# Kernel tuning notes

Measured on AMD Instinct MI355X. Metric: run time of the kernel, lower is better.

The kernel has to match this reference:

```python
import jax, jax.numpy as jnp
import numpy as np

D = 1280      # embed_dim
H = 20        # num_heads
HD = D // H   # head_dim = 64
B = 4         # batch (number of requests)
ENC = 1500    # encoder length per request (Whisper 30s)
KV = B * ENC  # 6000 packed cross kv tokens
SEQ = [300, 500, 350, 450]  # ragged decoder lengths, sum = 1600
Q = sum(SEQ)


def setup_inputs() -> dict:
    key = jax.random.key(0)
    ks = jax.random.split(key, 8)
    s = 0.02
    return {
        "hidden_states": jax.random.normal(ks[0], (Q, D), jnp.float32),
        "cross_hidden_states": jax.random.normal(ks[1], (KV, D), jnp.float32),
        "seq_lens": jnp.array(SEQ, dtype=jnp.int32),
        "Wq": jax.random.normal(ks[2], (D, D), jnp.float32) * s,
        "bq": jax.random.normal(ks[3], (D,), jnp.float32) * s,
        "Wkv": jax.random.normal(ks[4], (D, 2 * D), jnp.float32) * s,
        "bkv": jax.random.normal(ks[5], (2 * D,), jnp.float32) * s,
        "Wo": jax.random.normal(ks[6], (D, D), jnp.float32) * s,
        "bo": jax.random.normal(ks[7], (D,), jnp.float32) * s,
    }


def reference(hidden_states, cross_hidden_states, seq_lens, Wq, bq, Wkv, bkv, Wo, bo):
    q_len, d = hidden_states.shape
    kv_len = cross_hidden_states.shape[0]
    bsz = seq_lens.shape[0]
    enc_len = kv_len // bsz
    scaling = jnp.float32(HD) ** -0.5

    # projections (packed tokens)
    q = (hidden_states @ Wq + bq) * scaling           # [Q, D]
    kv = cross_hidden_states @ Wkv + bkv              # [KV, 2D]
    k, v = kv[:, :d], kv[:, d:]

    # [H, L, HD]
    qh = q.reshape(q_len, H, HD).transpose(1, 0, 2)
    kh = k.reshape(kv_len, H, HD).transpose(1, 0, 2)
    vh = v.reshape(kv_len, H, HD).transpose(1, 0, 2)

    scores = jnp.einsum("hqd,hkd->hqk", qh, kh)       # [H, Q, KV]

    # ragged block-diagonal mask: query token i belongs to request
    # searchsorted(cumsum(seq_lens), i, 'right'); kv token j to j // enc_len
    cum = jnp.cumsum(seq_lens)
    q_req = jnp.searchsorted(cum, jnp.arange(q_len), side="right")
    kv_req = jnp.arange(kv_len) // enc_len
    mask = q_req[:, None] == kv_req[None, :]          # [Q, KV] bool

    scores = jnp.where(mask[None, :, :], scores, -jnp.inf)
    probs = jax.nn.softmax(scores, axis=-1)
    attn = jnp.einsum("hqk,hkd->hqd", probs, vh)      # [H, Q, HD]
    attn = attn.transpose(1, 0, 2).reshape(q_len, d)
    return attn @ Wo + bo
```

## Files before the change

### kernel.cpp

```cpp
#include <hip/hip_runtime.h>
#include <stdint.h>

#define AS1 __attribute__((address_space(1)))
#define AS3 __attribute__((address_space(3)))

typedef __bf16 bf16_t;
typedef bf16_t bf16x8 __attribute__((ext_vector_type(8)));
typedef float  f32x4  __attribute__((ext_vector_type(4)));
typedef float  f32x16 __attribute__((ext_vector_type(16)));
typedef unsigned short u16;

constexpr int D     = 1280;
constexpr int H     = 20;
constexpr int HD    = 64;
constexpr int NQ    = 1600;
constexpr int NKV   = 6000;
constexpr int ENC   = 1500;
constexpr int QPAD  = 1632;
constexpr int KVP   = 1504;
constexpr int KVTOT = 4 * KVP;
constexpr int KB_PER_REQ = KVP / 32;
constexpr int KB_TOT     = 4 * KB_PER_REQ;

__device__ __forceinline__ u16 f2bf(float f) {
  union { float f; uint32_t u; } x; x.f = f;
  uint32_t r = (x.u + 0x7fffu + ((x.u >> 16) & 1u)) >> 16;
  return (u16)r;
}

__device__ __forceinline__ void gload16(const void* g, void* l) {
  __builtin_amdgcn_global_load_lds((AS1 void*)g, (AS3 void*)l, 16, 0, 0);
}

__device__ __forceinline__ void cvt_body(const float* __restrict__ in, u16* __restrict__ out,
                                         int i, int n4) {
  if (i >= n4) return;
  float4 v = ((const float4*)in)[i];
  ushort4 o;
  o.x = f2bf(v.x); o.y = f2bf(v.y); o.z = f2bf(v.z); o.w = f2bf(v.w);
  ((ushort4*)out)[i] = o;
}

__device__ __forceinline__ void tpose_body(const float* __restrict__ in, u16* __restrict__ out,
                                           int R, int C, int bx, int by, u16 (*tile)[33]) {
  int bc = bx * 32, br = by * 32;
  int tx = threadIdx.x & 31, ty = threadIdx.x >> 5;
#pragma unroll
  for (int i = 0; i < 32; i += 8)
    tile[ty + i][tx] = f2bf(in[(size_t)(br + ty + i) * C + bc + tx]);
  __syncthreads();
#pragma unroll
  for (int i = 0; i < 32; i += 8)
    out[(size_t)(bc + ty + i) * R + br + tx] = tile[tx][ty + i];
}

__global__ __launch_bounds__(256)
void prep_kernel(const float* __restrict__ hs, const float* __restrict__ chs,
                 const float* __restrict__ Wq, const float* __restrict__ Wkv,
                 const float* __restrict__ Wo,
                 u16* __restrict__ hsb, u16* __restrict__ chsb,
                 u16* __restrict__ Wqt, u16* __restrict__ Wkvt, u16* __restrict__ Wot) {
  __shared__ u16 tile[32][33];
  int b = blockIdx.x;
  if (b < 2000) {
    cvt_body(hs, hsb, b * 256 + threadIdx.x, 512000);
  } else if (b < 9500) {
    cvt_body(chs, chsb, (b - 2000) * 256 + threadIdx.x, 1920000);
  } else if (b < 11100) {
    int t = b - 9500;  tpose_body(Wq,  Wqt,  1280, 1280, t % 40, t / 40, tile);
  } else if (b < 14300) {
    int t = b - 11100; tpose_body(Wkv, Wkvt, 1280, 2560, t % 80, t / 80, tile);
  } else {
    int t = b - 14300; tpose_body(Wo,  Wot,  1280, 1280, t % 40, t / 40, tile);
  }
}

template <int MODE>
__device__ __forceinline__ void gemm_tile(
    int m0, int n0, const u16* __restrict__ A, const u16* __restrict__ Bt,
    const float* __restrict__ bias, int M,
    u16* __restrict__ outA, u16* __restrict__ outB, float* __restrict__ outF,
    u16* lds) {
  const int tid = threadIdx.x;
  const int lane = tid & 63, l15 = lane & 15, lg = lane >> 4;
  const int w = tid >> 6, wr = w >> 1, wc = w & 1;
  const bool vside = (MODE == 1) && (n0 >= D);
  constexpr int NT = D / 64;

  auto stage = [&](int tj, int c) {
    int buf = (tj & 1) * 32768;
    if (c < 4) {
      int off = c * 4096 + tid * 16;
      int loff = off ^ (((off >> 7) & 7) << 4);
      int row = loff >> 7, colb = loff & 127;
      int gr = m0 + row; gr = gr < M ? gr : M - 1;
      gload16((const char*)A + ((size_t)gr * D + tj * 64) * 2 + colb,
              (char*)lds + buf + off);
    } else {
      int off = (c - 4) * 4096 + tid * 16;
      int loff = off ^ (((off >> 7) & 7) << 4);
      int row = loff >> 7, colb = loff & 127;
      int gr = n0 + row;
      gload16((const char*)Bt + ((size_t)gr * D + tj * 64) * 2 + colb,
              (char*)lds + buf + 16384 + off);
    }
  };

  f32x4 acc[4][4] = {};

#pragma unroll
  for (int c = 0; c < 8; ++c) stage(0, c);
  asm volatile("s_waitcnt vmcnt(0)" ::: "memory");
  __builtin_amdgcn_s_barrier();
  __builtin_amdgcn_sched_barrier(0);

  for (int t = 0; t < NT; ++t) {
    if (t + 1 < NT) {
#pragma unroll
      for (int c = 0; c < 8; ++c) stage(t + 1, c);
    }
    __builtin_amdgcn_sched_barrier(0);

    const char* base = (const char*)lds + (t & 1) * 32768;
    bf16x8 af[4][2], bfr[4][2];
#pragma unroll
    for (int m = 0; m < 4; ++m)
#pragma unroll
      for (int kh = 0; kh < 2; ++kh) {
        int row = wr * 64 + m * 16 + l15;
        int bo = (row << 7) + kh * 64 + lg * 16;
        af[m][kh] = *(const bf16x8*)(base + (bo ^ ((row & 7) << 4)));
      }
#pragma unroll
    for (int n = 0; n < 4; ++n)
#pragma unroll
      for (int kh = 0; kh < 2; ++kh) {
        int row = wc * 64 + n * 16 + l15;
        int bo = (row << 7) + kh * 64 + lg * 16;
        bfr[n][kh] = *(const bf16x8*)(base + 16384 + (bo ^ ((row & 7) << 4)));
      }
    __builtin_amdgcn_s_setprio(1);
#pragma unroll
    for (int m = 0; m < 4; ++m)
#pragma unroll
      for (int n = 0; n < 4; ++n)
#pragma unroll
        for (int kh = 0; kh < 2; ++kh)
          acc[m][n] = vside
            ? __builtin_amdgcn_mfma_f32_16x16x32_bf16(bfr[n][kh], af[m][kh], acc[m][n], 0, 0, 0)
            : __builtin_amdgcn_mfma_f32_16x16x32_bf16(af[m][kh], bfr[n][kh], acc[m][n], 0, 0, 0);
    __builtin_amdgcn_s_setprio(0);

    if (t + 1 < NT) {
      asm volatile("s_waitcnt vmcnt(0)" ::: "memory");
      __builtin_amdgcn_s_barrier();
      __builtin_amdgcn_sched_barrier(0);
    }
  }

  if (!vside) {
#pragma unroll
    for (int m = 0; m < 4; ++m)
#pragma unroll
      for (int n = 0; n < 4; ++n) {
        int col = n0 + wc * 64 + n * 16 + l15;
        float bv = bias[col];
#pragma unroll
        for (int r = 0; r < 4; ++r) {
          int row = m0 + wr * 64 + m * 16 + lg * 4 + r;
          if (row >= M) continue;
          float v = acc[m][n][r] + bv;
          if (MODE == 0) {
            v *= 0.125f;
            int h = col >> 6, hd = col & 63;
            outA[((size_t)(h * QPAD + row)) * HD + hd] = f2bf(v);
          } else if (MODE == 1) {
            int req = row / ENC, loc = row - req * ENC;
            int rr = req * KVP + loc;
            int h = col >> 6, hd = col & 63;
            int kb2 = rr >> 5, kv = rr & 31;
            outA[((size_t)((h * KB_TOT + kb2) * 4 + (hd >> 4))) * 512 + kv * 16 + (hd & 15)] = f2bf(v);
          } else {
            outF[(size_t)row * D + col] = v;
          }
        }
      }
  } else {
    float bvv[4][4];
#pragma unroll
    for (int n = 0; n < 4; ++n)
#pragma unroll
      for (int r = 0; r < 4; ++r)
        bvv[n][r] = bias[n0 + wc * 64 + n * 16 + lg * 4 + r];
#pragma unroll
    for (int m = 0; m < 4; ++m) {
      int gm = m0 + wr * 64 + m * 16 + l15;
      int req = gm / ENC, loc = gm - req * ENC;
      int rr = req * KVP + loc;
      int kb2 = rr >> 5, kv = rr & 31;
      bool ok = gm < M;
#pragma unroll
      for (int n = 0; n < 4; ++n)
#pragma unroll
        for (int r = 0; r < 4; ++r) {
          if (!ok) continue;
          int c2 = n0 + wc * 64 + n * 16 + lg * 4 + r - D;
          int h = c2 >> 6, hd = c2 & 63;
          outB[((size_t)((h * KB_TOT + kb2) * 64 + hd)) * 32 + kv] = f2bf(acc[m][n][r] + bvv[n][r]);
        }
    }
  }
}

__global__ __launch_bounds__(256)
void qkv_gemm_kernel(const u16* __restrict__ hsb, const u16* __restrict__ chsb,
                     const u16* __restrict__ Wqt, const u16* __restrict__ Wkvt,
                     const float* __restrict__ bq, const float* __restrict__ bkv,
                     u16* __restrict__ qhb, u16* __restrict__ khb, u16* __restrict__ vtb) {
  __shared__ __align__(16) u16 lds[32768];
  const int nwg = 1070, q8 = nwg >> 3, r8 = nwg & 7;
  const int xcd = blockIdx.x & 7, pos = blockIdx.x >> 3;
  const int wg = (xcd < r8 ? xcd * (q8 + 1) : r8 * (q8 + 1) + (xcd - r8) * q8) + pos;
  if (wg < 940) {
    gemm_tile<1>((wg / 20) * 128, (wg % 20) * 128, chsb, Wkvt, bkv, NKV,
                 khb, vtb, nullptr, lds);
  } else {
    int w2 = wg - 940;
    gemm_tile<0>((w2 / 10) * 128, (w2 % 10) * 128, hsb, Wqt, bq, NQ,
                 qhb, nullptr, nullptr, lds);
  }
}

__global__ __launch_bounds__(256)
void o_gemm_kernel(const u16* __restrict__ attnb, const u16* __restrict__ Wot,
                   const float* __restrict__ bo, float* __restrict__ out) {
  __shared__ __align__(16) u16 lds[32768];
  const int nwg = 130, q8 = nwg >> 3, r8 = nwg & 7;
  const int xcd = blockIdx.x & 7, pos = blockIdx.x >> 3;
  const int wg = (xcd < r8 ? xcd * (q8 + 1) : r8 * (q8 + 1) + (xcd - r8) * q8) + pos;
  gemm_tile<2>((wg / 10) * 128, (wg % 10) * 128, attnb, Wot, bo, NQ,
               nullptr, nullptr, out, lds);
}

__global__ __launch_bounds__(256)
void attn_kernel(const u16* __restrict__ kbuf, const u16* __restrict__ vbuf,
                 const u16* __restrict__ qh, const int* __restrict__ seq,
                 u16* __restrict__ attnb) {
  __shared__ __align__(16) float smem[4][2176];
  const int lane = threadIdx.x & 63;
  const int l31 = lane & 31, h5 = lane >> 5;
  const int w = threadIdx.x >> 6;

  const int xcd = blockIdx.x & 7, pos = blockIdx.x >> 3;
  const int g = xcd * 160 + pos;
  const int p = g >> 4, t = g & 15;
  const int head = p >> 2, req = p & 3;

  int s0 = seq[0], s1 = seq[1], s2 = seq[2];
  int qstart = (req > 0 ? s0 : 0) + (req > 1 ? s1 : 0) + (req > 2 ? s2 : 0);
  int slen = seq[req];
  int q0 = t * 32;
  if (q0 >= slen) return;

  const u16* qrow = qh + ((size_t)(head * QPAD + qstart + q0 + l31)) * HD + h5 * 8;
  bf16x8 qb[4];
#pragma unroll
  for (int ks = 0; ks < 4; ++ks) qb[ks] = *(const bf16x8*)(qrow + ks * 16);

  const u16* kpan = kbuf + (size_t)(head * KB_TOT + req * KB_PER_REQ) * 2048 + l31 * 16 + h5 * 8;
  const u16* vpan = vbuf + (size_t)(head * KB_TOT + req * KB_PER_REQ) * 2048 + l31 * 32 + h5 * 8;
  const float C = 1.44269504088896340736f;

  f32x16 o0 = {}, o1 = {};
  float mx = -__builtin_inff(), ls = 0.f;

  const int kvs = w * 384;
  const int kve = (w == 3) ? ENC : kvs + 384;

  bf16x8 ka[4], va[2][2], kan[4], van[2][2];
  {
    const u16* kp = kpan + (size_t)(kvs >> 5) * 2048;
    const u16* vp = vpan + (size_t)(kvs >> 5) * 2048;
#pragma unroll
    for (int ks = 0; ks < 4; ++ks) ka[ks] = *(const bf16x8*)(kp + ks * 512);
#pragma unroll
    for (int dt = 0; dt < 2; ++dt)
#pragma unroll
      for (int ks = 0; ks < 2; ++ks)
        va[dt][ks] = *(const bf16x8*)(vp + dt * 1024 + ks * 16);
  }

  for (int kvb = kvs; kvb < kve; kvb += 32) {
    int nb = (kvb + 32 < kve ? kvb + 32 : kvs) >> 5;
    {
      const u16* kp = kpan + (size_t)nb * 2048;
      const u16* vp = vpan + (size_t)nb * 2048;
#pragma unroll
      for (int ks = 0; ks < 4; ++ks) kan[ks] = *(const bf16x8*)(kp + ks * 512);
#pragma unroll
      for (int dt = 0; dt < 2; ++dt)
#pragma unroll
        for (int ks = 0; ks < 2; ++ks)
          van[dt][ks] = *(const bf16x8*)(vp + dt * 1024 + ks * 16);
    }

    f32x16 sa = {};
    __builtin_amdgcn_s_setprio(1);
#pragma unroll
    for (int ks = 0; ks < 4; ++ks)
      sa = __builtin_amdgcn_mfma_f32_32x32x16_bf16(ka[ks], qb[ks], sa, 0, 0, 0);
    __builtin_amdgcn_s_setprio(0);

    if (kvb + 32 > ENC) {
#pragma unroll
      for (int r = 0; r < 16; ++r) {
        int kvr = (r & 3) + 4 * h5 + 8 * (r >> 2);
        sa[r] = (kvb + kvr >= ENC) ? -__builtin_inff() : sa[r];
      }
    }

    float tm = sa[0];
#pragma unroll
    for (int r = 1; r < 16; ++r) tm = fmaxf(tm, sa[r]);
    tm = fmaxf(tm, __shfl_xor(tm, 32));

    if (__any(tm > mx + 8.0f)) {
      float mnew = fmaxf(mx, tm);
      float sc = exp2f((mx - mnew) * C);
      mx = mnew;
      ls *= sc;
      o0 *= sc; o1 *= sc;
    }
    float psum = 0.f;
#pragma unroll
    for (int r = 0; r < 16; ++r) { sa[r] = exp2f((sa[r] - mx) * C); psum += sa[r]; }
    ls += psum;

    uint32_t a[8], x[8];
#pragma unroll
    for (int i = 0; i < 8; ++i)
      a[i] = (uint32_t)f2bf(sa[2 * i]) | ((uint32_t)f2bf(sa[2 * i + 1]) << 16);
#pragma unroll
    for (int i = 0; i < 8; ++i) x[i] = (uint32_t)__shfl_xor((int)a[i], 32);
    union { uint32_t w4[4]; bf16x8 v; } pb0, pb1;
    pb0.w4[0] = h5 ? x[2] : a[0]; pb0.w4[1] = h5 ? x[3] : a[1];
    pb0.w4[2] = h5 ? a[2] : x[0]; pb0.w4[3] = h5 ? a[3] : x[1];
    pb1.w4[0] = h5 ? x[6] : a[4]; pb1.w4[1] = h5 ? x[7] : a[5];
    pb1.w4[2] = h5 ? a[6] : x[4]; pb1.w4[3] = h5 ? a[7] : x[5];

    __builtin_amdgcn_s_setprio(1);
    o0 = __builtin_amdgcn_mfma_f32_32x32x16_bf16(va[0][0], pb0.v, o0, 0, 0, 0);
    o0 = __builtin_amdgcn_mfma_f32_32x32x16_bf16(va[0][1], pb1.v, o0, 0, 0, 0);
    o1 = __builtin_amdgcn_mfma_f32_32x32x16_bf16(va[1][0], pb0.v, o1, 0, 0, 0);
    o1 = __builtin_amdgcn_mfma_f32_32x32x16_bf16(va[1][1], pb1.v, o1, 0, 0, 0);
    __builtin_amdgcn_s_setprio(0);

#pragma unroll
    for (int ks = 0; ks < 4; ++ks) ka[ks] = kan[ks];
#pragma unroll
    for (int dt = 0; dt < 2; ++dt)
#pragma unroll
      for (int ks = 0; ks < 2; ++ks) va[dt][ks] = van[dt][ks];
  }

  ls += __shfl_xor(ls, 32);

#pragma unroll
  for (int r = 0; r < 16; ++r) {
    int drow = (r & 3) + 8 * (r >> 2) + 4 * h5;
    smem[w][drow * 33 + l31] = o0[r];
    smem[w][(drow + 32) * 33 + l31] = o1[r];
  }
  if (h5 == 0) {
    smem[w][2112 + l31] = mx;
    smem[w][2144 + l31] = ls;
  }
  __syncthreads();

#pragma unroll
  for (int it = 0; it < 8; ++it) {
    int item = threadIdx.x + it * 256;
    int q = item >> 6, d = item & 63;
    float m0v = smem[0][2112 + q], m1v = smem[1][2112 + q];
    float m2v = smem[2][2112 + q], m3v = smem[3][2112 + q];
    float M = fmaxf(fmaxf(m0v, m1v), fmaxf(m2v, m3v));
    float e0 = exp2f((m0v - M) * C), e1 = exp2f((m1v - M) * C);
    float e2 = exp2f((m2v - M) * C), e3 = exp2f((m3v - M) * C);
    float L = smem[0][2144 + q] * e0 + smem[1][2144 + q] * e1 +
              smem[2][2144 + q] * e2 + smem[3][2144 + q] * e3;
    float O = smem[0][d * 33 + q] * e0 + smem[1][d * 33 + q] * e1 +
              smem[2][d * 33 + q] * e2 + smem[3][d * 33 + q] * e3;
    int qr = q0 + q;
    if (qr < slen)
      attnb[(size_t)(qstart + qr) * D + head * HD + d] = f2bf(O / L);
  }
}

extern "C" void kernel_launch(void* const* d_in, const int* in_sizes, int n_in,
                              void* d_out, int out_size, void* d_ws, size_t ws_size,
                              hipStream_t stream) {
  const float* hs  = (const float*)d_in[0];
  const float* chs = (const float*)d_in[1];
  const int*   seq = (const int*)d_in[2];
  const float* Wq  = (const float*)d_in[3];
  const float* bq  = (const float*)d_in[4];
  const float* Wkv = (const float*)d_in[5];
  const float* bkv = (const float*)d_in[6];
  const float* Wo  = (const float*)d_in[7];
  const float* bo  = (const float*)d_in[8];

  char* ws = (char*)d_ws;
  u16* hsb   = (u16*)(ws + 0);
  u16* chsb  = (u16*)(ws + 4096000);
  u16* Wqt   = (u16*)(ws + 19456000);
  u16* Wkvt  = (u16*)(ws + 22732800);
  u16* Wot   = (u16*)(ws + 29286400);
  u16* qhb   = (u16*)(ws + 32563200);
  u16* khb   = (u16*)(ws + 36741120);
  u16* vtb   = (u16*)(ws + 52142080);
  u16* attnb = (u16*)(ws + 67543040);

  prep_kernel<<<15900, 256, 0, stream>>>(hs, chs, Wq, Wkv, Wo, hsb, chsb, Wqt, Wkvt, Wot);
  qkv_gemm_kernel<<<1070, 256, 0, stream>>>(hsb, chsb, Wqt, Wkvt, bq, bkv, qhb, khb, vtb);
  attn_kernel<<<1280, 256, 0, stream>>>(khb, vtb, qhb, seq, attnb);
  o_gemm_kernel<<<130, 256, 0, stream>>>(attnb, Wot, bo, (float*)d_out);
}
```

Before: 169.4 us.

## Use 128x256 tiles with 32x32 MFMA and single-buffered LDS in GEMMs

Reworks the shared GEMM tile to cover 128x256 outputs per block using 32x32x16 bf16 MFMA instructions, with each wave computing a 64x128 sub-tile. The double-buffered prefetch pipeline is replaced by a single LDS buffer guarded by syncthreads, which reduces LDS use. Grid sizes for the QKV and output GEMMs are halved to match. The aim is more operand reuse per LDS read and fewer MFMA issues, at the cost of losing load/compute overlap and running far fewer blocks on the output GEMM.

```diff
diff --git a/kernel.cpp b/kernel.cpp
--- a/kernel.cpp
+++ b/kernel.cpp
@@ -82,94 +82,72 @@
     u16* __restrict__ outA, u16* __restrict__ outB, float* __restrict__ outF,
     u16* lds) {
   const int tid = threadIdx.x;
-  const int lane = tid & 63, l15 = lane & 15, lg = lane >> 4;
-  const int w = tid >> 6, wr = w >> 1, wc = w & 1;
+  const int lane = tid & 63, l31 = lane & 31, h5 = lane >> 5;
+  const int w = tid >> 6, wm = w >> 1, wn = w & 1;
   const bool vside = (MODE == 1) && (n0 >= D);
-  constexpr int NT = D / 64;
-
-  auto stage = [&](int tj, int c) {
-    int buf = (tj & 1) * 32768;
-    if (c < 4) {
+  u16* As = lds;
+  u16* Bs = lds + 8192;
+
+  f32x16 acc[2][4] = {};
+
+  for (int t = 0; t < D / 64; ++t) {
+#pragma unroll
+    for (int c = 0; c < 4; ++c) {
       int off = c * 4096 + tid * 16;
       int loff = off ^ (((off >> 7) & 7) << 4);
       int row = loff >> 7, colb = loff & 127;
       int gr = m0 + row; gr = gr < M ? gr : M - 1;
-      gload16((const char*)A + ((size_t)gr * D + tj * 64) * 2 + colb,
-              (char*)lds + buf + off);
-    } else {
-      int off = (c - 4) * 4096 + tid * 16;
+      gload16((const char*)A + ((size_t)gr * D + t * 64) * 2 + colb, (char*)As + off);
+    }
+#pragma unroll
+    for (int c = 0; c < 8; ++c) {
+      int off = c * 4096 + tid * 16;
       int loff = off ^ (((off >> 7) & 7) << 4);
       int row = loff >> 7, colb = loff & 127;
-      int gr = n0 + row;
-      gload16((const char*)Bt + ((size_t)gr * D + tj * 64) * 2 + colb,
-              (char*)lds + buf + 16384 + off);
-    }
-  };
-
-  f32x4 acc[4][4] = {};
-
-#pragma unroll
-  for (int c = 0; c < 8; ++c) stage(0, c);
-  asm volatile("s_waitcnt vmcnt(0)" ::: "memory");
-  __builtin_amdgcn_s_barrier();
-  __builtin_amdgcn_sched_barrier(0);
-
-  for (int t = 0; t < NT; ++t) {
-    if (t + 1 < NT) {
-#pragma unroll
-      for (int c = 0; c < 8; ++c) stage(t + 1, c);
-    }
-    __builtin_amdgcn_sched_barrier(0);
-
-    const char* base = (const char*)lds + (t & 1) * 32768;
-    bf16x8 af[4][2], bfr[4][2];
-#pragma unroll
-    for (int m = 0; m < 4; ++m)
-#pragma unroll
-      for (int kh = 0; kh < 2; ++kh) {
-        int row = wr * 64 + m * 16 + l15;
-        int bo = (row << 7) + kh * 64 + lg * 16;
-        af[m][kh] = *(const bf16x8*)(base + (bo ^ ((row & 7) << 4)));
+      gload16((const char*)Bt + ((size_t)(n0 + row) * D + t * 64) * 2 + colb, (char*)Bs + off);
+    }
+    __syncthreads();
+
+#pragma unroll
+    for (int ks = 0; ks < 4; ++ks) {
+      bf16x8 af[2], bfr[4];
+#pragma unroll
+      for (int fm = 0; fm < 2; ++fm) {
+        int row = wm * 64 + fm * 32 + l31;
+        int bo = (row << 7) + ks * 32 + h5 * 16;
+        af[fm] = *(const bf16x8*)((const char*)As + (bo ^ ((row & 7) << 4)));
       }
 #pragma unroll
-    for (int n = 0; n < 4; ++n)
-#pragma unroll
-      for (int kh = 0; kh < 2; ++kh) {
-        int row = wc * 64 + n * 16 + l15;
-        int bo = (row << 7) + kh * 64 + lg * 16;
-        bfr[n][kh] = *(const bf16x8*)(base + 16384 + (bo ^ ((row & 7) << 4)));
+      for (int fn = 0; fn < 4; ++fn) {
+        int row = wn * 128 + fn * 32 + l31;
+        int bo = (row << 7) + ks * 32 + h5 * 16;
+        bfr[fn] = *(const bf16x8*)((const char*)Bs + (bo ^ ((row & 7) << 4)));
       }
-    __builtin_amdgcn_s_setprio(1);
-#pragma unroll
-    for (int m = 0; m < 4; ++m)
-#pragma unroll
-      for (int n = 0; n < 4; ++n)
-#pragma unroll
-        for (int kh = 0; kh < 2; ++kh)
-          acc[m][n] = vside
-            ? __builtin_amdgcn_mfma_f32_16x16x32_bf16(bfr[n][kh], af[m][kh], acc[m][n], 0, 0, 0)
-            : __builtin_amdgcn_mfma_f32_16x16x32_bf16(af[m][kh], bfr[n][kh], acc[m][n], 0, 0, 0);
-    __builtin_amdgcn_s_setprio(0);
-
-    if (t + 1 < NT) {
-      asm volatile("s_waitcnt vmcnt(0)" ::: "memory");
-      __builtin_amdgcn_s_barrier();
-      __builtin_amdgcn_sched_barrier(0);
-    }
+      __builtin_amdgcn_s_setprio(1);
+#pragma unroll
+      for (int fm = 0; fm < 2; ++fm)
+#pragma unroll
+        for (int fn = 0; fn < 4; ++fn)
+          acc[fm][fn] = vside
+            ? __builtin_amdgcn_mfma_f32_32x32x16_bf16(bfr[fn], af[fm], acc[fm][fn], 0, 0, 0)
+            : __builtin_amdgcn_mfma_f32_32x32x16_bf16(af[fm], bfr[fn], acc[fm][fn], 0, 0, 0);
+      __builtin_amdgcn_s_setprio(0);
+    }
+    __syncthreads();
   }
 
   if (!vside) {
 #pragma unroll
-    for (int m = 0; m < 4; ++m)
-#pragma unroll
-      for (int n = 0; n < 4; ++n) {
-        int col = n0 + wc * 64 + n * 16 + l15;
+    for (int fm = 0; fm < 2; ++fm)
+#pragma unroll
+      for (int fn = 0; fn < 4; ++fn) {
+        int col = n0 + wn * 128 + fn * 32 + l31;
         float bv = bias[col];
 #pragma unroll
-        for (int r = 0; r < 4; ++r) {
-          int row = m0 + wr * 64 + m * 16 + lg * 4 + r;
+        for (int r = 0; r < 16; ++r) {
+          int row = m0 + wm * 64 + fm * 32 + (r & 3) + 8 * (r >> 2) + 4 * h5;
           if (row >= M) continue;
-          float v = acc[m][n][r] + bv;
+          float v = acc[fm][fn][r] + bv;
           if (MODE == 0) {
             v *= 0.125f;
             int h = col >> 6, hd = col & 63;
@@ -186,27 +164,22 @@
         }
       }
   } else {
-    float bvv[4][4];
-#pragma unroll
-    for (int n = 0; n < 4; ++n)
-#pragma unroll
-      for (int r = 0; r < 4; ++r)
-        bvv[n][r] = bias[n0 + wc * 64 + n * 16 + lg * 4 + r];
-#pragma unroll
-    for (int m = 0; m < 4; ++m) {
-      int gm = m0 + wr * 64 + m * 16 + l15;
+#pragma unroll
+    for (int fm = 0; fm < 2; ++fm) {
+      int gm = m0 + wm * 64 + fm * 32 + l31;
       int req = gm / ENC, loc = gm - req * ENC;
       int rr = req * KVP + loc;
       int kb2 = rr >> 5, kv = rr & 31;
       bool ok = gm < M;
 #pragma unroll
-      for (int n = 0; n < 4; ++n)
-#pragma unroll
-        for (int r = 0; r < 4; ++r) {
+      for (int fn = 0; fn < 4; ++fn)
+#pragma unroll
+        for (int r = 0; r < 16; ++r) {
           if (!ok) continue;
-          int c2 = n0 + wc * 64 + n * 16 + lg * 4 + r - D;
+          int c2 = n0 + wn * 128 + fn * 32 + (r & 3) + 8 * (r >> 2) + 4 * h5 - D;
           int h = c2 >> 6, hd = c2 & 63;
-          outB[((size_t)((h * KB_TOT + kb2) * 64 + hd)) * 32 + kv] = f2bf(acc[m][n][r] + bvv[n][r]);
+          outB[((size_t)((h * KB_TOT + kb2) * 64 + hd)) * 32 + kv] =
+              f2bf(acc[fm][fn][r] + bias[c2 + D]);
         }
     }
   }
@@ -217,16 +190,16 @@
                      const u16* __restrict__ Wqt, const u16* __restrict__ Wkvt,
                      const float* __restrict__ bq, const float* __restrict__ bkv,
                      u16* __restrict__ qhb, u16* __restrict__ khb, u16* __restrict__ vtb) {
-  __shared__ __align__(16) u16 lds[32768];
-  const int nwg = 1070, q8 = nwg >> 3, r8 = nwg & 7;
+  __shared__ __align__(16) u16 lds[24576];
+  const int nwg = 535, q8 = nwg >> 3, r8 = nwg & 7;
   const int xcd = blockIdx.x & 7, pos = blockIdx.x >> 3;
   const int wg = (xcd < r8 ? xcd * (q8 + 1) : r8 * (q8 + 1) + (xcd - r8) * q8) + pos;
-  if (wg < 940) {
-    gemm_tile<1>((wg / 20) * 128, (wg % 20) * 128, chsb, Wkvt, bkv, NKV,
+  if (wg < 470) {
+    gemm_tile<1>((wg / 10) * 128, (wg % 10) * 256, chsb, Wkvt, bkv, NKV,
                  khb, vtb, nullptr, lds);
   } else {
-    int w2 = wg - 940;
-    gemm_tile<0>((w2 / 10) * 128, (w2 % 10) * 128, hsb, Wqt, bq, NQ,
+    int w2 = wg - 470;
+    gemm_tile<0>((w2 / 5) * 128, (w2 % 5) * 256, hsb, Wqt, bq, NQ,
                  qhb, nullptr, nullptr, lds);
   }
 }
@@ -234,11 +207,11 @@
 __global__ __launch_bounds__(256)
 void o_gemm_kernel(const u16* __restrict__ attnb, const u16* __restrict__ Wot,
                    const float* __restrict__ bo, float* __restrict__ out) {
-  __shared__ __align__(16) u16 lds[32768];
-  const int nwg = 130, q8 = nwg >> 3, r8 = nwg & 7;
+  __shared__ __align__(16) u16 lds[24576];
+  const int nwg = 65, q8 = nwg >> 3, r8 = nwg & 7;
   const int xcd = blockIdx.x & 7, pos = blockIdx.x >> 3;
   const int wg = (xcd < r8 ? xcd * (q8 + 1) : r8 * (q8 + 1) + (xcd - r8) * q8) + pos;
-  gemm_tile<2>((wg / 10) * 128, (wg % 10) * 128, attnb, Wot, bo, NQ,
+  gemm_tile<2>((wg / 5) * 128, (wg % 5) * 256, attnb, Wot, bo, NQ,
                nullptr, nullptr, out, lds);
 }
 
@@ -421,7 +394,7 @@
   u16* attnb = (u16*)(ws + 67543040);
 
   prep_kernel<<<15900, 256, 0, stream>>>(hs, chs, Wq, Wkv, Wo, hsb, chsb, Wqt, Wkvt, Wot);
-  qkv_gemm_kernel<<<1070, 256, 0, stream>>>(hsb, chsb, Wqt, Wkvt, bq, bkv, qhb, khb, vtb);
+  qkv_gemm_kernel<<<535, 256, 0, stream>>>(hsb, chsb, Wqt, Wkvt, bq, bkv, qhb, khb, vtb);
   attn_kernel<<<1280, 256, 0, stream>>>(khb, vtb, qhb, seq, attnb);
-  o_gemm_kernel<<<130, 256, 0, stream>>>(attnb, Wot, bo, (float*)d_out);
-}
+  o_gemm_kernel<<<65, 256, 0, stream>>>(attnb, Wot, bo, (float*)d_out);
+}
```

After: 273.1 us. 1.61x slower.
